# Performance work log

Measured on AMD Instinct MI355X. Metric: run time of the kernel, lower is better.

The kernel has to match this reference:

```python
import jax, jax.numpy as jnp
import numpy as np

B, S, D, H = 4, 2048, 512, 8
HD = D // H  # head_size = 64


def setup_inputs() -> dict:
    key = jax.random.key(0)
    ks = jax.random.split(key, 11)
    sd = 1.0 / np.sqrt(D)
    return {
        "q": jax.random.normal(ks[0], (B, S, D), jnp.float32),
        "k": jax.random.normal(ks[1], (B, S, D), jnp.float32),
        "v": jax.random.normal(ks[2], (B, S, D), jnp.float32),
        "Wq": jax.random.normal(ks[3], (D, D), jnp.float32) * sd,
        "bq": jnp.zeros((D,), jnp.float32),
        "Wk": jax.random.normal(ks[4], (D, D), jnp.float32) * sd,
        "bk": jnp.zeros((D,), jnp.float32),
        "Wv": jax.random.normal(ks[5], (D, D), jnp.float32) * sd,
        "bv": jnp.zeros((D,), jnp.float32),
        "Wo": jax.random.normal(ks[6], (D, D), jnp.float32) * sd,
        "bo": jnp.zeros((D,), jnp.float32),
    }


def _split_heads(x):
    # [B,S,D] -> [B,H,S,HD]
    return x.reshape(B, S, H, HD).transpose(0, 2, 1, 3)


def reference(q, k, v, Wq, bq, Wk, bk, Wv, bv, Wo, bo):
    qp = _split_heads(q @ Wq.T + bq)
    kp = _split_heads(k @ Wk.T + bk)
    vp = _split_heads(v @ Wv.T + bv)
    scale = 1.0 / jnp.sqrt(jnp.float32(HD))
    scores = jnp.einsum("bhqd,bhkd->bhqk", qp, kp) * scale  # [B,H,S,S]
    weights = jax.nn.softmax(scores, axis=-1)
    ctx = jnp.einsum("bhqk,bhkd->bhqd", weights, vp)
    ctx = ctx.transpose(0, 2, 1, 3).reshape(B, S, D)
    return ctx @ Wo.T + bo
```

## Files before the change

kernel.cpp:

```cpp
#include <hip/hip_runtime.h>
#include <hip/hip_bf16.h>
#include <stdint.h>

#define BB   4
#define SS   2048
#define DDIM 512
#define HH   8
#define HDIM 64
#define MTOT (BB*SS)
#define QSCALE (0.125f * 1.44269504088896340736f)

typedef __bf16 bf16;
typedef __bf16 bf16x8 __attribute__((ext_vector_type(8)));
typedef float  f32x4  __attribute__((ext_vector_type(4)));

__device__ __forceinline__ f32x4 mfma32(bf16x8 a, bf16x8 b, f32x4 c) {
    return __builtin_amdgcn_mfma_f32_16x16x32_bf16(a, b, c, 0, 0, 0);
}

__device__ __forceinline__ void gload_lds16(const void* g, void* l) {
    __builtin_amdgcn_global_load_lds(
        (__attribute__((address_space(1))) unsigned int*)(uintptr_t)g,
        (__attribute__((address_space(3))) unsigned int*)l,
        16, 0, 0);
}

__device__ __forceinline__ short bf16bits(float f) {
    union { __bf16 h; short s; } u; u.h = (__bf16)f; return u.s;
}

__global__ void cvt_kernel(const float* __restrict__ q, const float* __restrict__ k,
                           const float* __restrict__ v, const float* __restrict__ w0,
                           const float* __restrict__ w1, const float* __restrict__ w2,
                           const float* __restrict__ w3,
                           bf16* __restrict__ dq, bf16* __restrict__ dk,
                           bf16* __restrict__ dv, bf16* __restrict__ dw0,
                           bf16* __restrict__ dw1, bf16* __restrict__ dw2,
                           bf16* __restrict__ dw3) {
    const float* s; bf16* d; int n4;
    switch (blockIdx.y) {
        case 0: s = q;  d = dq;  n4 = (BB*SS*DDIM)/4; break;
        case 1: s = k;  d = dk;  n4 = (BB*SS*DDIM)/4; break;
        case 2: s = v;  d = dv;  n4 = (BB*SS*DDIM)/4; break;
        case 3: s = w0; d = dw0; n4 = (DDIM*DDIM)/4; break;
        case 4: s = w1; d = dw1; n4 = (DDIM*DDIM)/4; break;
        case 5: s = w2; d = dw2; n4 = (DDIM*DDIM)/4; break;
        default: s = w3; d = dw3; n4 = (DDIM*DDIM)/4; break;
    }
    int stride = gridDim.x * blockDim.x;
    for (int i = blockIdx.x * blockDim.x + threadIdx.x; i < n4; i += stride) {
        float4 f = ((const float4*)s)[i];
        union { bf16 h[4]; uint2 u; } o;
        o.h[0] = (bf16)f.x; o.h[1] = (bf16)f.y; o.h[2] = (bf16)f.z; o.h[3] = (bf16)f.w;
        ((uint2*)d)[i] = o.u;
    }
}

#define GEMM_CORE(A_, W_, K_, MB_, NB_)                                          \
    __shared__ bf16 As[2][128 * 32];                                             \
    __shared__ bf16 Bs[2][128 * 32];                                             \
    const int tid = threadIdx.x;                                                 \
    const int w = tid >> 6, lane = tid & 63;                                     \
    const int c15 = lane & 15, quad = lane >> 4;                                 \
    const int mblk = (MB_), nblk = (NB_);                                        \
    const int wm = (w & 1) * 64, wn = (w >> 1) * 64;                             \
    f32x4 acc[4][4] = {};                                                        \
    const bf16* Ab = (A_) + (size_t)mblk * (K_);                                 \
    const bf16* Bb = (W_) + (size_t)nblk * (K_);                                 \
    int goff[2], soff[2];                                                        \
    _Pragma("unroll")                                                            \
    for (int ci = 0; ci < 2; ++ci) {                                             \
        const int s = (w * 2 + ci) * 64 + lane;                 \
        const int kr = s >> 2;                                                   \
        const int c = (s & 3) ^ ((kr >> 1) & 3);                                 \
        goff[ci] = kr * (K_) + c * 8;                                            \
        soff[ci] = s * 8;                                                        \
    }                                                                            \
    _Pragma("unroll")                                                            \
    for (int ci = 0; ci < 2; ++ci) {                                             \
        gload_lds16(Ab + goff[ci], &As[0][soff[ci]]);                            \
        gload_lds16(Bb + goff[ci], &Bs[0][soff[ci]]);                            \
    }                                                                            \
    int bufi = 0;                                                                \
    for (int kt = 0; kt < (K_); kt += 32) {                                      \
        __syncthreads();              \
        if (kt + 32 < (K_)) {                                                    \
            _Pragma("unroll")                                                    \
            for (int ci = 0; ci < 2; ++ci) {                                     \
                gload_lds16(Ab + goff[ci] + kt + 32, &As[bufi ^ 1][soff[ci]]);   \
                gload_lds16(Bb + goff[ci] + kt + 32, &Bs[bufi ^ 1][soff[ci]]);   \
            }                                                                    \
        }                                                                        \
        bf16x8 af[4], bfr[4];                                                    \
        _Pragma("unroll")                                                        \
        for (int i = 0; i < 4; ++i) {                                            \
            const int row = wm + i * 16 + c15;                                   \
            af[i] = *(const bf16x8*)&As[bufi][row * 32 + ((quad ^ ((row >> 1) & 3)) * 8)]; \
        }                                                                        \
        _Pragma("unroll")                                                        \
        for (int j = 0; j < 4; ++j) {                                            \
            const int row = wn + j * 16 + c15;                                   \
            bfr[j] = *(const bf16x8*)&Bs[bufi][row * 32 + ((quad ^ ((row >> 1) & 3)) * 8)]; \
        }                                                                        \
        _Pragma("unroll")                                                        \
        for (int i = 0; i < 4; ++i)                                              \
            _Pragma("unroll")                                                    \
            for (int j = 0; j < 4; ++j)                                          \
                acc[i][j] = mfma32(af[i], bfr[j], acc[i][j]);                    \
        bufi ^= 1;                                                               \
    }

__global__ __launch_bounds__(256, 4)
void proj_gemm(const bf16* __restrict__ qb, const bf16* __restrict__ kb,
               const bf16* __restrict__ vb,
               const bf16* __restrict__ Wq, const bf16* __restrict__ Wk,
               const bf16* __restrict__ Wv,
               const float* __restrict__ bq, const float* __restrict__ bk,
               const float* __restrict__ bv,
               bf16* __restrict__ Qp, bf16* __restrict__ Kp, bf16* __restrict__ Vt2) {
    const int mode = blockIdx.z;
    const bf16* A; const bf16* Wm; const float* bias;
    int mb, nb;
    if (mode == 0)      { A = qb; Wm = Wq; bias = bq; mb = blockIdx.x * 128; nb = blockIdx.y * 128; }
    else if (mode == 1) { A = kb; Wm = Wk; bias = bk; mb = blockIdx.x * 128; nb = blockIdx.y * 128; }
    else {
        const int id = blockIdx.y * 64 + blockIdx.x;
        A = Wv; Wm = vb; bias = bv; mb = (id & 3) * 128; nb = (id >> 2) * 128;
    }
    GEMM_CORE(A, Wm, DDIM, mb, nb)
    if (mode == 2) {
        #pragma unroll
        for (int i = 0; i < 4; ++i) {
            #pragma unroll
            for (int r = 0; r < 4; ++r) {
                const int row = mblk + wm + i * 16 + quad * 4 + r;
                const float bval = bias[row];
                #pragma unroll
                for (int j = 0; j < 4; ++j) {
                    const int col = nblk + wn + j * 16 + c15;
                    const int colp = (col & ~31) + (c15 >> 2) * 8 + (j & 1) * 4 + (c15 & 3);
                    Vt2[(size_t)row * MTOT + colp] = (bf16)(acc[i][j][r] + bval);
                }
            }
        }
    } else {
        #pragma unroll
        for (int j = 0; j < 4; ++j) {
            const int col = nblk + wn + j * 16 + c15;
            const int h = col >> 6, hd = col & 63;
            const float bval = bias[col];
            #pragma unroll
            for (int i = 0; i < 4; ++i) {
                #pragma unroll
                for (int r = 0; r < 4; ++r) {
                    const int row = mblk + wm + i * 16 + quad * 4 + r;
                    const int b = row >> 11, s = row & (SS - 1);
                    float vv = acc[i][j][r] + bval;
                    if (mode == 0) vv *= QSCALE;
                    bf16* dst = (mode == 0) ? Qp : Kp;
                    dst[(((size_t)(b * HH + h)) * SS + s) * HDIM + hd] = (bf16)vv;
                }
            }
        }
    }
}

__global__ __launch_bounds__(256, 4)
void out_gemm(const bf16* __restrict__ A, const bf16* __restrict__ Wo,
              const float* __restrict__ bo, float* __restrict__ Out) {
    GEMM_CORE(A, Wo, DDIM, blockIdx.x * 128, blockIdx.y * 128)
    #pragma unroll
    for (int j = 0; j < 4; ++j) {
        const int col = nblk + wn + j * 16 + c15;
        const float bval = bo[col];
        #pragma unroll
        for (int i = 0; i < 4; ++i) {
            #pragma unroll
            for (int r = 0; r < 4; ++r) {
                const int row = mblk + wm + i * 16 + quad * 4 + r;
                Out[(size_t)row * DDIM + col] = acc[i][j][r] + bval;
            }
        }
    }
}

__global__ __launch_bounds__(256, 2)
void attn_kernel(const bf16* __restrict__ Qp, const bf16* __restrict__ Kp,
                 const bf16* __restrict__ Vt2, bf16* __restrict__ Ctx) {
    __shared__ bf16 Klds[2][128 * 64];
    __shared__ bf16 Vlds[2][64 * 128];

    const int tid = threadIdx.x;
    const int w = tid >> 6, lane = tid & 63;
    const int c15 = lane & 15, quad = lane >> 4;
    const int id = blockIdx.y * 16 + blockIdx.x;
    const int bh = id & 31;
    const int qbase = (id >> 5) * 128;
    const int b = bh >> 3, h = bh & 7;

    const bf16* Qh = Qp + (size_t)bh * SS * HDIM;
    const bf16* Kh = Kp + (size_t)bh * SS * HDIM;
    const bf16* Vh = Vt2 + (size_t)h * HDIM * MTOT + (size_t)b * SS;

    bf16x8 qf[2][2];
    #pragma unroll
    for (int g = 0; g < 2; ++g) {
        const int qrow = qbase + w * 32 + g * 16 + c15;
        qf[g][0] = *(const bf16x8*)&Qh[(size_t)qrow * HDIM + quad * 8];
        qf[g][1] = *(const bf16x8*)&Qh[(size_t)qrow * HDIM + 32 + quad * 8];
    }

    int koff[4], voff[4];
    #pragma unroll
    for (int ci = 0; ci < 4; ++ci) {
        const int s = (w * 4 + ci) * 64 + lane;
        const int kr = s >> 3, kc = (s & 7) ^ (kr & 7);
        koff[ci] = kr * HDIM + kc * 8;
        const int vr = s >> 4, vc = (s & 15) ^ (vr & 15);
        voff[ci] = vr * MTOT + vc * 8;
    }

    union FragS { short s[8]; bf16x8 v; };
    FragS ones8;
    #pragma unroll
    for (int j = 0; j < 8; ++j) ones8.s[j] = (short)0x3F80;

    f32x4 oacc[2][4] = {};
    f32x4 lacc[2] = {};
    const int ksw = c15 & 7;

    #pragma unroll
    for (int ci = 0; ci < 4; ++ci) {
        gload_lds16(Kh + koff[ci], &Klds[0][(w * 4 + ci) * 512]);
        gload_lds16(Vh + voff[ci], &Vlds[0][(w * 4 + ci) * 512]);
    }

    int buf = 0;
    for (int kt = 0; kt < SS; kt += 128) {
        __syncthreads();
        if (kt + 128 < SS) {
            const bf16* Ks = Kh + (size_t)(kt + 128) * HDIM;
            const bf16* Vs = Vh + (kt + 128);
            #pragma unroll
            for (int ci = 0; ci < 4; ++ci) {
                gload_lds16(Ks + koff[ci], &Klds[buf ^ 1][(w * 4 + ci) * 512]);
                gload_lds16(Vs + voff[ci], &Vlds[buf ^ 1][(w * 4 + ci) * 512]);
            }
        }

        FragS paf[2][4];
        #pragma unroll
        for (int nt = 0; nt < 8; ++nt) {
            const int krow = nt * 16 + c15;
            bf16x8 kb0 = *(const bf16x8*)&Klds[buf][(krow * 8 + (quad ^ ksw)) * 8];
            bf16x8 kb1 = *(const bf16x8*)&Klds[buf][(krow * 8 + ((quad + 4) ^ ksw)) * 8];
            #pragma unroll
            for (int g = 0; g < 2; ++g) {
                f32x4 z = {};
                z = mfma32(kb0, qf[g][0], z);
                z = mfma32(kb1, qf[g][1], z);
                const int half = (nt & 1) * 4;
                #pragma unroll
                for (int r = 0; r < 4; ++r)
                    paf[g][nt >> 1].s[half + r] =
                        bf16bits(__builtin_amdgcn_exp2f(z[r]));
            }
        }

        #pragma unroll
        for (int t = 0; t < 4; ++t) {
            bf16x8 vbf[4];
            #pragma unroll
            for (int j = 0; j < 4; ++j) {
                const int row = j * 16 + c15;
                vbf[j] = *(const bf16x8*)&Vlds[buf][row * 128 +
                         (((4 * t + quad) ^ c15) * 8)];
            }
            __builtin_amdgcn_s_setprio(1);
            lacc[0] = mfma32(paf[0][t].v, ones8.v, lacc[0]);
            lacc[1] = mfma32(paf[1][t].v, ones8.v, lacc[1]);
            #pragma unroll
            for (int j = 0; j < 4; ++j) {
                oacc[0][j] = mfma32(paf[0][t].v, vbf[j], oacc[0][j]);
                oacc[1][j] = mfma32(paf[1][t].v, vbf[j], oacc[1][j]);
            }
            __builtin_amdgcn_s_setprio(0);
        }
        buf ^= 1;
    }

    bf16* Cb = Ctx + ((size_t)b * SS) * DDIM + (size_t)h * HDIM;
    #pragma unroll
    for (int g = 0; g < 2; ++g)
        #pragma unroll
        for (int r = 0; r < 4; ++r) {
            const int row = qbase + w * 32 + g * 16 + quad * 4 + r;
            const float inv = 1.0f / lacc[g][r];
            #pragma unroll
            for (int j = 0; j < 4; ++j) {
                const int hd = j * 16 + c15;
                Cb[(size_t)row * DDIM + hd] = (bf16)(oacc[g][j][r] * inv);
            }
        }
}

extern "C" void kernel_launch(void* const* d_in, const int* in_sizes, int n_in,
                              void* d_out, int out_size, void* d_ws, size_t ws_size,
                              hipStream_t stream) {
    const float* q  = (const float*)d_in[0];
    const float* k  = (const float*)d_in[1];
    const float* v  = (const float*)d_in[2];
    const float* Wq = (const float*)d_in[3];
    const float* bq = (const float*)d_in[4];
    const float* Wk = (const float*)d_in[5];
    const float* bk = (const float*)d_in[6];
    const float* Wv = (const float*)d_in[7];
    const float* bv = (const float*)d_in[8];
    const float* Wo = (const float*)d_in[9];
    const float* bo = (const float*)d_in[10];
    float* out = (float*)d_out;

    const size_t SZ_T = (size_t)BB * SS * DDIM * 2;
    const size_t SZ_W = (size_t)DDIM * DDIM * 2;
    char* ws = (char*)d_ws;
    bf16* qb  = (bf16*)(ws + 0 * SZ_T);
    bf16* kb  = (bf16*)(ws + 1 * SZ_T);
    bf16* vb  = (bf16*)(ws + 2 * SZ_T);
    bf16* Wqb = (bf16*)(ws + 3 * SZ_T + 0 * SZ_W);
    bf16* Wkb = (bf16*)(ws + 3 * SZ_T + 1 * SZ_W);
    bf16* Wvb = (bf16*)(ws + 3 * SZ_T + 2 * SZ_W);
    bf16* Wob = (bf16*)(ws + 3 * SZ_T + 3 * SZ_W);
    bf16* Qp  = (bf16*)(ws + 3 * SZ_T + 4 * SZ_W);
    bf16* Kp  = (bf16*)(ws + 4 * SZ_T + 4 * SZ_W);
    bf16* Vt2 = (bf16*)(ws + 5 * SZ_T + 4 * SZ_W);
    bf16* ctx = (bf16*)(ws + 6 * SZ_T + 4 * SZ_W);
    const size_t needed = 7 * SZ_T + 4 * SZ_W;
    if (ws_size < needed) return;

    cvt_kernel<<<dim3(512, 7), 256, 0, stream>>>(q, k, v, Wq, Wk, Wv, Wo,
                                                 qb, kb, vb, Wqb, Wkb, Wvb, Wob);
    proj_gemm<<<dim3(MTOT / 128, DDIM / 128, 3), 256, 0, stream>>>(
        qb, kb, vb, Wqb, Wkb, Wvb, bq, bk, bv, Qp, Kp, Vt2);
    attn_kernel<<<dim3(SS / 128, BB * HH), 256, 0, stream>>>(Qp, Kp, Vt2, ctx);
    out_gemm<<<dim3(MTOT / 128, DDIM / 128), 256, 0, stream>>>(ctx, Wob, bo, out);
}
```

Baseline: 176.8 us.

## Load V fragments directly from global memory into registers instead of LDS

Drops the double-buffered LDS staging of V. Each lane now loads its own V^T fragments straight from global memory at the start of each key tile, ahead of the QK^T compute, so the load latency overlaps that compute. This halves LDS use per block and removes the swizzled LDS reads for V. In exchange each wave redundantly fetches the same V data, with 64 extra VGPRs per lane, more global and L2 traffic, and a risk of exposed memory latency.

```diff
diff --git a/kernel.cpp b/kernel.cpp
--- a/kernel.cpp
+++ b/kernel.cpp
@@ -188,7 +188,6 @@
 void attn_kernel(const bf16* __restrict__ Qp, const bf16* __restrict__ Kp,
                  const bf16* __restrict__ Vt2, bf16* __restrict__ Ctx) {
     __shared__ bf16 Klds[2][128 * 64];
-    __shared__ bf16 Vlds[2][64 * 128];
 
     const int tid = threadIdx.x;
     const int w = tid >> 6, lane = tid & 63;
@@ -210,15 +209,18 @@
         qf[g][1] = *(const bf16x8*)&Qh[(size_t)qrow * HDIM + 32 + quad * 8];
     }
 
-    int koff[4], voff[4];
+    int koff[4];
     #pragma unroll
     for (int ci = 0; ci < 4; ++ci) {
         const int s = (w * 4 + ci) * 64 + lane;
         const int kr = s >> 3, kc = (s & 7) ^ (kr & 7);
         koff[ci] = kr * HDIM + kc * 8;
-        const int vr = s >> 4, vc = (s & 15) ^ (vr & 15);
-        voff[ci] = vr * MTOT + vc * 8;
-    }
+    }
+
+    const bf16* vrow[4];
+    #pragma unroll
+    for (int j = 0; j < 4; ++j)
+        vrow[j] = Vh + (size_t)(j * 16 + c15) * MTOT + quad * 8;
 
     union FragS { short s[8]; bf16x8 v; };
     FragS ones8;
@@ -230,22 +232,25 @@
     const int ksw = c15 & 7;
 
     #pragma unroll
-    for (int ci = 0; ci < 4; ++ci) {
+    for (int ci = 0; ci < 4; ++ci)
         gload_lds16(Kh + koff[ci], &Klds[0][(w * 4 + ci) * 512]);
-        gload_lds16(Vh + voff[ci], &Vlds[0][(w * 4 + ci) * 512]);
-    }
 
     int buf = 0;
     for (int kt = 0; kt < SS; kt += 128) {
         __syncthreads();
+
+        bf16x8 vv[4][4];
+        #pragma unroll
+        for (int t = 0; t < 4; ++t)
+            #pragma unroll
+            for (int j = 0; j < 4; ++j)
+                vv[t][j] = *(const bf16x8*)(vrow[j] + kt + 32 * t);
+
         if (kt + 128 < SS) {
             const bf16* Ks = Kh + (size_t)(kt + 128) * HDIM;
-            const bf16* Vs = Vh + (kt + 128);
-            #pragma unroll
-            for (int ci = 0; ci < 4; ++ci) {
+            #pragma unroll
+            for (int ci = 0; ci < 4; ++ci)
                 gload_lds16(Ks + koff[ci], &Klds[buf ^ 1][(w * 4 + ci) * 512]);
-                gload_lds16(Vs + voff[ci], &Vlds[buf ^ 1][(w * 4 + ci) * 512]);
-            }
         }
 
         FragS paf[2][4];
@@ -269,20 +274,13 @@
 
         #pragma unroll
         for (int t = 0; t < 4; ++t) {
-            bf16x8 vbf[4];
-            #pragma unroll
-            for (int j = 0; j < 4; ++j) {
-                const int row = j * 16 + c15;
-                vbf[j] = *(const bf16x8*)&Vlds[buf][row * 128 +
-                         (((4 * t + quad) ^ c15) * 8)];
-            }
             __builtin_amdgcn_s_setprio(1);
             lacc[0] = mfma32(paf[0][t].v, ones8.v, lacc[0]);
             lacc[1] = mfma32(paf[1][t].v, ones8.v, lacc[1]);
             #pragma unroll
             for (int j = 0; j < 4; ++j) {
-                oacc[0][j] = mfma32(paf[0][t].v, vbf[j], oacc[0][j]);
-                oacc[1][j] = mfma32(paf[1][t].v, vbf[j], oacc[1][j]);
+                oacc[0][j] = mfma32(paf[0][t].v, vv[t][j], oacc[0][j]);
+                oacc[1][j] = mfma32(paf[1][t].v, vv[t][j], oacc[1][j]);
             }
             __builtin_amdgcn_s_setprio(0);
         }
```

Measured after the change: 213.0 us. 1.2x slower.

## Halve attention query tile and single-buffer V to raise occupancy

Applied to the files above, without the earlier changes.

The attention kernel now handles 64 query rows per block (16 per wave) instead of 128, doubling the grid. The V tile becomes single-buffered: it is loaded at the start of each iteration, while the QK/exp stage runs, and a second barrier is added before the PV stage. Launch bounds move from 2 to 3 blocks per SIMD. The goal is lower LDS and register use per block and more resident waves to hide latency. The cost is that each K/V tile and each K fragment is reused by half as many queries, which doubles K/V load traffic. V load latency is also only partly hidden, and the extra barrier adds a sync per iteration.

```diff
diff --git a/kernel.cpp b/kernel.cpp
--- a/kernel.cpp
+++ b/kernel.cpp
@@ -184,31 +184,27 @@
     }
 }
 
-__global__ __launch_bounds__(256, 2)
+__global__ __launch_bounds__(256, 3)
 void attn_kernel(const bf16* __restrict__ Qp, const bf16* __restrict__ Kp,
                  const bf16* __restrict__ Vt2, bf16* __restrict__ Ctx) {
     __shared__ bf16 Klds[2][128 * 64];
-    __shared__ bf16 Vlds[2][64 * 128];
+    __shared__ bf16 Vlds[64 * 128];
 
     const int tid = threadIdx.x;
     const int w = tid >> 6, lane = tid & 63;
     const int c15 = lane & 15, quad = lane >> 4;
-    const int id = blockIdx.y * 16 + blockIdx.x;
+    const int id = blockIdx.y * 32 + blockIdx.x;
     const int bh = id & 31;
-    const int qbase = (id >> 5) * 128;
+    const int qbase = (id >> 5) * 64;
     const int b = bh >> 3, h = bh & 7;
 
     const bf16* Qh = Qp + (size_t)bh * SS * HDIM;
     const bf16* Kh = Kp + (size_t)bh * SS * HDIM;
     const bf16* Vh = Vt2 + (size_t)h * HDIM * MTOT + (size_t)b * SS;
 
-    bf16x8 qf[2][2];
-    #pragma unroll
-    for (int g = 0; g < 2; ++g) {
-        const int qrow = qbase + w * 32 + g * 16 + c15;
-        qf[g][0] = *(const bf16x8*)&Qh[(size_t)qrow * HDIM + quad * 8];
-        qf[g][1] = *(const bf16x8*)&Qh[(size_t)qrow * HDIM + 32 + quad * 8];
-    }
+    const int qrow = qbase + w * 16 + c15;
+    const bf16x8 qf0 = *(const bf16x8*)&Qh[(size_t)qrow * HDIM + quad * 8];
+    const bf16x8 qf1 = *(const bf16x8*)&Qh[(size_t)qrow * HDIM + 32 + quad * 8];
 
     int koff[4], voff[4];
     #pragma unroll
@@ -225,47 +221,48 @@
     #pragma unroll
     for (int j = 0; j < 8; ++j) ones8.s[j] = (short)0x3F80;
 
-    f32x4 oacc[2][4] = {};
-    f32x4 lacc[2] = {};
+    f32x4 oacc[4] = {};
+    f32x4 lacc = {};
     const int ksw = c15 & 7;
 
     #pragma unroll
     for (int ci = 0; ci < 4; ++ci) {
         gload_lds16(Kh + koff[ci], &Klds[0][(w * 4 + ci) * 512]);
-        gload_lds16(Vh + voff[ci], &Vlds[0][(w * 4 + ci) * 512]);
+        gload_lds16(Vh + voff[ci], &Vlds[(w * 4 + ci) * 512]);
     }
 
     int buf = 0;
     for (int kt = 0; kt < SS; kt += 128) {
         __syncthreads();
+        if (kt > 0) {
+            const bf16* Vs = Vh + kt;
+            #pragma unroll
+            for (int ci = 0; ci < 4; ++ci)
+                gload_lds16(Vs + voff[ci], &Vlds[(w * 4 + ci) * 512]);
+        }
         if (kt + 128 < SS) {
             const bf16* Ks = Kh + (size_t)(kt + 128) * HDIM;
-            const bf16* Vs = Vh + (kt + 128);
-            #pragma unroll
-            for (int ci = 0; ci < 4; ++ci) {
+            #pragma unroll
+            for (int ci = 0; ci < 4; ++ci)
                 gload_lds16(Ks + koff[ci], &Klds[buf ^ 1][(w * 4 + ci) * 512]);
-                gload_lds16(Vs + voff[ci], &Vlds[buf ^ 1][(w * 4 + ci) * 512]);
-            }
-        }
-
-        FragS paf[2][4];
+        }
+
+        FragS paf[4];
         #pragma unroll
         for (int nt = 0; nt < 8; ++nt) {
             const int krow = nt * 16 + c15;
             bf16x8 kb0 = *(const bf16x8*)&Klds[buf][(krow * 8 + (quad ^ ksw)) * 8];
             bf16x8 kb1 = *(const bf16x8*)&Klds[buf][(krow * 8 + ((quad + 4) ^ ksw)) * 8];
-            #pragma unroll
-            for (int g = 0; g < 2; ++g) {
-                f32x4 z = {};
-                z = mfma32(kb0, qf[g][0], z);
-                z = mfma32(kb1, qf[g][1], z);
-                const int half = (nt & 1) * 4;
-                #pragma unroll
-                for (int r = 0; r < 4; ++r)
-                    paf[g][nt >> 1].s[half + r] =
-                        bf16bits(__builtin_amdgcn_exp2f(z[r]));
-            }
-        }
+            f32x4 z = {};
+            z = mfma32(kb0, qf0, z);
+            z = mfma32(kb1, qf1, z);
+            const int half = (nt & 1) * 4;
+            #pragma unroll
+            for (int r = 0; r < 4; ++r)
+                paf[nt >> 1].s[half + r] = bf16bits(__builtin_amdgcn_exp2f(z[r]));
+        }
+
+        __syncthreads();
 
         #pragma unroll
         for (int t = 0; t < 4; ++t) {
@@ -273,17 +270,13 @@
             #pragma unroll
             for (int j = 0; j < 4; ++j) {
                 const int row = j * 16 + c15;
-                vbf[j] = *(const bf16x8*)&Vlds[buf][row * 128 +
-                         (((4 * t + quad) ^ c15) * 8)];
+                vbf[j] = *(const bf16x8*)&Vlds[row * 128 + (((4 * t + quad) ^ c15) * 8)];
             }
             __builtin_amdgcn_s_setprio(1);
-            lacc[0] = mfma32(paf[0][t].v, ones8.v, lacc[0]);
-            lacc[1] = mfma32(paf[1][t].v, ones8.v, lacc[1]);
-            #pragma unroll
-            for (int j = 0; j < 4; ++j) {
-                oacc[0][j] = mfma32(paf[0][t].v, vbf[j], oacc[0][j]);
-                oacc[1][j] = mfma32(paf[1][t].v, vbf[j], oacc[1][j]);
-            }
+            lacc = mfma32(paf[t].v, ones8.v, lacc);
+            #pragma unroll
+            for (int j = 0; j < 4; ++j)
+                oacc[j] = mfma32(paf[t].v, vbf[j], oacc[j]);
             __builtin_amdgcn_s_setprio(0);
         }
         buf ^= 1;
@@ -291,17 +284,15 @@
 
     bf16* Cb = Ctx + ((size_t)b * SS) * DDIM + (size_t)h * HDIM;
     #pragma unroll
-    for (int g = 0; g < 2; ++g)
-        #pragma unroll
-        for (int r = 0; r < 4; ++r) {
-            const int row = qbase + w * 32 + g * 16 + quad * 4 + r;
-            const float inv = 1.0f / lacc[g][r];
-            #pragma unroll
-            for (int j = 0; j < 4; ++j) {
-                const int hd = j * 16 + c15;
-                Cb[(size_t)row * DDIM + hd] = (bf16)(oacc[g][j][r] * inv);
-            }
-        }
+    for (int r = 0; r < 4; ++r) {
+        const int row = qbase + w * 16 + quad * 4 + r;
+        const float inv = 1.0f / lacc[r];
+        #pragma unroll
+        for (int j = 0; j < 4; ++j) {
+            const int hd = j * 16 + c15;
+            Cb[(size_t)row * DDIM + hd] = (bf16)(oacc[j][r] * inv);
+        }
+    }
 }
 
 extern "C" void kernel_launch(void* const* d_in, const int* in_sizes, int n_in,
@@ -341,6 +332,6 @@
                                                  qb, kb, vb, Wqb, Wkb, Wvb, Wob);
     proj_gemm<<<dim3(MTOT / 128, DDIM / 128, 3), 256, 0, stream>>>(
         qb, kb, vb, Wqb, Wkb, Wvb, bq, bk, bv, Qp, Kp, Vt2);
-    attn_kernel<<<dim3(SS / 128, BB * HH), 256, 0, stream>>>(Qp, Kp, Vt2, ctx);
+    attn_kernel<<<dim3(SS / 64, BB * HH), 256, 0, stream>>>(Qp, Kp, Vt2, ctx);
     out_gemm<<<dim3(MTOT / 128, DDIM / 128), 256, 0, stream>>>(ctx, Wob, bo, out);
 }
```

New measurement: 185.1 us. +4.7%, slower.
